# Kernel tuning notes

Measured on AMD Instinct MI355X. Metric: run time of the kernel, lower is better.

Reference implementation:

```python
import jax, jax.numpy as jnp
import numpy as np

B = 32768
STATE_DIM = 5
MEAS_DIM = 4
CTRL_DIM = 2
HIDDEN = 128
NOISE_HIDDEN = 64
DT = 0.01
Q_ENTR_LB = 7.1
N_SIG = 2 * STATE_DIM + 1
LAM = 3.0 - STATE_DIM          # merwe kappa = 3 - n, alpha = 1, beta = 0
C = STATE_DIM + LAM            # = 3.0


def _ukf_weights():
    wm = jnp.full((N_SIG,), 1.0 / (2.0 * C), dtype=jnp.float32)
    return wm.at[0].set(LAM / C)


def _sigma_points(x, P):
    # x: [B,n], P: [B,n,n] -> [B, 2n+1, n]
    L = jnp.linalg.cholesky(C * P)
    cols = jnp.swapaxes(L, -1, -2)  # row i is the i-th column of L
    return jnp.concatenate([x[:, None, :], x[:, None, :] + cols, x[:, None, :] - cols], axis=1)


def _dyn(xu, W1, b1, W2, b2):
    # ODE right-hand side on the augmented state xu: [B, S, state+ctrl]
    return jnp.tanh(xu @ W1 + b1) @ W2 + b2


def _rk4(xu, W1, b1, W2, b2):
    # single RK4 step over dt (odeint(model, xu, dt)[-1])
    f = lambda z: _dyn(z, W1, b1, W2, b2)
    k1 = f(xu)
    k2 = f(xu + 0.5 * DT * k1)
    k3 = f(xu + 0.5 * DT * k2)
    k4 = f(xu + DT * k3)
    return xu + (DT / 6.0) * (k1 + 2.0 * k2 + 2.0 * k3 + k4)


def _entropy(M):
    D = M.shape[-1]
    return 0.5 * D * (1.0 + jnp.log(2.0 * jnp.pi)) + 0.5 * jnp.linalg.slogdet(M)[1]


def setup_inputs() -> dict:
    key = jax.random.key(0)
    ks = jax.random.split(key, 12)
    d_in = STATE_DIM + CTRL_DIM
    X_hat = jax.random.normal(ks[0], (B, STATE_DIM), dtype=jnp.float32)
    A = 0.1 * jax.random.normal(ks[1], (B, STATE_DIM, STATE_DIM), dtype=jnp.float32)
    P = A @ jnp.swapaxes(A, -1, -2) + 0.1 * jnp.eye(STATE_DIM, dtype=jnp.float32)  # SPD
    u = jax.random.normal(ks[2], (B, CTRL_DIM), dtype=jnp.float32)
    y = jax.random.normal(ks[3], (B, MEAS_DIM), dtype=jnp.float32)
    W1 = 0.05 * jax.random.normal(ks[4], (d_in, HIDDEN), dtype=jnp.float32)
    b1 = jnp.zeros((HIDDEN,), dtype=jnp.float32)
    W2 = 0.05 * jax.random.normal(ks[5], (HIDDEN, d_in), dtype=jnp.float32)
    b2 = jnp.zeros((d_in,), dtype=jnp.float32)
    Wn1 = 0.05 * jax.random.normal(ks[6], (STATE_DIM, NOISE_HIDDEN), dtype=jnp.float32)
    bn1 = jnp.zeros((NOISE_HIDDEN,), dtype=jnp.float32)
    Wq = 0.05 * jax.random.normal(ks[7], (NOISE_HIDDEN, STATE_DIM), dtype=jnp.float32)
    bq = jnp.zeros((STATE_DIM,), dtype=jnp.float32)
    Wr = 0.05 * jax.random.normal(ks[8], (NOISE_HIDDEN, MEAS_DIM), dtype=jnp.float32)
    br = jnp.zeros((MEAS_DIM,), dtype=jnp.float32)
    Hobs = 0.3 * jax.random.normal(ks[9], (d_in, MEAS_DIM), dtype=jnp.float32)
    return {"X_hat": X_hat, "P": P, "u": u, "y": y,
            "W1": W1, "b1": b1, "W2": W2, "b2": b2,
            "Wn1": Wn1, "bn1": bn1, "Wq": Wq, "bq": bq, "Wr": Wr, "br": br,
            "Hobs": Hobs}


def reference(X_hat, P, u, y, W1, b1, W2, b2, Wn1, bn1, Wq, bq, Wr, br, Hobs):
    wm = _ukf_weights()
    wc = wm  # alpha=1, beta=0 -> Wc0 == Wm0
    # --- noise model: per-sample diagonal Q, R from a small MLP ---
    h = jnp.tanh(X_hat @ Wn1 + bn1)
    Q = jnp.eye(STATE_DIM, dtype=X_hat.dtype) * jnp.exp(h @ Wq + bq)[:, :, None]
    R = jnp.eye(MEAS_DIM, dtype=X_hat.dtype) * jnp.exp(h @ Wr + br)[:, :, None]
    # --- entropy projection on Q (boolean mask -> where) ---
    ent_q = _entropy(Q)
    scale = jnp.where(ent_q < Q_ENTR_LB, jnp.exp((Q_ENTR_LB - ent_q) / STATE_DIM), 1.0)
    Q = scale[:, None, None] * Q
    ur = jnp.broadcast_to(u[:, None, :], (u.shape[0], N_SIG, CTRL_DIM))
    # --- UKF predict ---
    pts = _sigma_points(X_hat, P)                       # [B,11,5]
    xu = jnp.concatenate([pts, ur], axis=-1)            # [B,11,7]
    pts_n = _rk4(xu, W1, b1, W2, b2)[..., :STATE_DIM]   # integrate, keep state dims
    x_pred = jnp.einsum('s,bsn->bn', wm, pts_n)
    d = pts_n - x_pred[:, None, :]
    P_pred = jnp.einsum('s,bsi,bsj->bij', wc, d, d) + Q
    # --- UKF update ---
    pts2 = _sigma_points(x_pred, P_pred)
    Y = jnp.concatenate([pts2, ur], axis=-1) @ Hobs     # [B,11,4]
    y_hat = jnp.einsum('s,bsm->bm', wm, Y)
    dy = Y - y_hat[:, None, :]
    S = jnp.einsum('s,bsi,bsj->bij', wc, dy, dy) + R
    dx = pts2 - x_pred[:, None, :]
    Pxy = jnp.einsum('s,bsi,bsj->bij', wc, dx, dy)
    # K = Pxy @ S^{-1}, via solve (S symmetric)
    K = jnp.swapaxes(jnp.linalg.solve(S, jnp.swapaxes(Pxy, -1, -2)), -1, -2)
    X_new = x_pred + jnp.einsum('bij,bj->bi', K, y - y_hat)
    P_new = P_pred - K @ S @ jnp.swapaxes(K, -1, -2)
    return (X_new, P_new, _entropy(Q), _entropy(R))
```

## Files before the change

kernel.cpp:

```cpp
#include <hip/hip_runtime.h>
#include <math.h>

#define B_N   32768
#define SD    5
#define MD    4
#define HID   128
#define NH    64
#define DT    0.01f

#define IDX(i, j) ((i) * ((i) + 1) / 2 + (j))

typedef _Float16 h2v  __attribute__((ext_vector_type(2)));
typedef float    f32x4 __attribute__((ext_vector_type(4)));

#define CONST_AS __attribute__((address_space(4)))

__device__ __forceinline__ f32x4 ldc4(const float* p) {
    return *(const CONST_AS f32x4*)(uintptr_t)p;
}

__device__ __forceinline__ float fexp2(float x) {
#if __has_builtin(__builtin_amdgcn_exp2f)
    return __builtin_amdgcn_exp2f(x);
#else
    return exp2f(x);
#endif
}

__device__ __forceinline__ float fexp(float x) {
    return fexp2(x * 1.4426950408889634f);
}

__device__ __forceinline__ float packh2(float a, float b) {
    union { h2v h; float f; } u;
    u.h.x = (_Float16)a; u.h.y = (_Float16)b;
    return u.f;
}
__device__ __forceinline__ float unpk_lo(float f) {
    union { float f; h2v h; } u; u.f = f; return (float)u.h.x;
}
__device__ __forceinline__ float unpk_hi(float f) {
    union { float f; h2v h; } u; u.f = f; return (float)u.h.y;
}
__device__ __forceinline__ float pk_neg(float f) {
    union { float f; unsigned u; } x; x.f = f; x.u ^= 0x80008000u; return x.f;
}

__device__ __forceinline__ float pk_fma_vs(float a, float b_s, float c) {
    float d;
    asm("v_pk_fma_f16 %0, %1, %2, %3" : "=v"(d) : "v"(a), "s"(b_s), "v"(c));
    return d;
}
__device__ __forceinline__ float pk_fma_vv(float a, float b, float c) {
    float d;
    asm("v_pk_fma_f16 %0, %1, %2, %3" : "=v"(d) : "v"(a), "v"(b), "v"(c));
    return d;
}
__device__ __forceinline__ float pk_mul(float a, float b) {
    float d;
    asm("v_pk_mul_f16 %0, %1, %2" : "=v"(d) : "v"(a), "v"(b));
    return d;
}
__device__ __forceinline__ float pk_mul_vs(float a, float b_s) {
    float d;
    asm("v_pk_mul_f16 %0, %1, %2" : "=v"(d) : "v"(a), "s"(b_s));
    return d;
}
__device__ __forceinline__ float pk_add(float a, float b) {
    float d;
    asm("v_pk_add_f16 %0, %1, %2" : "=v"(d) : "v"(a), "v"(b));
    return d;
}
__device__ __forceinline__ float pk_max(float a, float b) {
    float d;
    asm("v_pk_max_f16 %0, %1, %2" : "=v"(d) : "v"(a), "v"(b));
    return d;
}
__device__ __forceinline__ float pk_min(float a, float b) {
    float d;
    asm("v_pk_min_f16 %0, %1, %2" : "=v"(d) : "v"(a), "v"(b));
    return d;
}

__device__ __forceinline__ float pk_tanh(float pre) {
    const float PHIc = packh2(3.0f, 3.0f);
    const float PLOc = packh2(-3.0f, -3.0f);
    const float C4c  = packh2(0.000412619f, 0.000412619f);
    const float C3c  = packh2(-0.00901606f, -0.00901606f);
    const float C2c  = packh2(0.07293188f, 0.07293188f);
    const float C1c  = packh2(-0.30093534f, -0.30093534f);
    const float C0c  = packh2(0.9982018f, 0.9982018f);
    float pc = pk_min(pk_max(pre, PLOc), PHIc);
    float u = pk_mul(pc, pc);
    float h = pk_fma_vv(u, C4c, C3c);
    h = pk_fma_vv(u, h, C2c);
    h = pk_fma_vv(u, h, C1c);
    h = pk_fma_vv(u, h, C0c);
    return pk_mul(pc, h);
}

__global__ void ukf_prep(const float* __restrict__ W1, const float* __restrict__ b1,
                         const float* __restrict__ W2,
                         const float* __restrict__ Wn1, const float* __restrict__ bn1,
                         const float* __restrict__ Wq, const float* __restrict__ Wr,
                         float* __restrict__ wpk, float* __restrict__ wnk) {
    const int p = threadIdx.x;
    if (p < 64) {
        const int k0 = 2 * p, k1 = 2 * p + 1;
        float* o = wpk + p * 16;
#pragma unroll
        for (int i = 0; i < 7; ++i) o[i] = packh2(W1[i * HID + k0], W1[i * HID + k1]);
        o[7] = packh2(b1[k0], b1[k1]);
#pragma unroll
        for (int j = 0; j < 7; ++j) o[8 + j] = packh2(W2[k0 * 7 + j], W2[k1 * 7 + j]);
        o[15] = 0.0f;
    } else if (p < 96) {
        const int q = p - 64;
        const int k0 = 2 * q, k1 = 2 * q + 1;
        float* o = wnk + q * 16;
#pragma unroll
        for (int i = 0; i < 5; ++i) o[i] = packh2(Wn1[i * NH + k0], Wn1[i * NH + k1]);
        o[5] = packh2(bn1[k0], bn1[k1]);
#pragma unroll
        for (int j = 0; j < 5; ++j) o[6 + j] = packh2(Wq[k0 * 5 + j], Wq[k1 * 5 + j]);
#pragma unroll
        for (int j = 0; j < 4; ++j) o[11 + j] = packh2(Wr[k0 * 4 + j], Wr[k1 * 4 + j]);
        o[15] = 0.0f;
    }
}

#define PSTR 259
__global__ __launch_bounds__(640) void ukf_main(
    const float* __restrict__ Xh, const float* __restrict__ Pin,
    const float* __restrict__ Uin, const float* __restrict__ Yin,
    const float* __restrict__ b2g, const float* __restrict__ bqg,
    const float* __restrict__ brg, const float* __restrict__ Hg,
    const float* __restrict__ wpk, const float* __restrict__ wnk,
    float* __restrict__ out) {
    __shared__ float part[64 * PSTR];

    const int tid = threadIdx.x;
    const int role = tid >> 6;
    const int e = tid & 63;
    const int bb = blockIdx.x * 64 + e;

    float x[SD];
#pragma unroll
    for (int i = 0; i < SD; ++i) x[i] = Xh[bb * SD + i];

    if (role < 8) {
        const float u0 = Uin[bb * 2 + 0];
        const float u1 = Uin[bb * 2 + 1];
        float zb[7];
#pragma unroll
        for (int i = 0; i < SD; ++i) zb[i] = packh2(x[i], x[i]);
        zb[5] = packh2(u0, u0);
        zb[6] = packh2(u1, u1);
        const float ONE2 = packh2(1.0f, 1.0f);

        float fb[5];
        float J2[25];
#pragma unroll
        for (int i = 0; i < 5; ++i) fb[i] = 0.0f;
#pragma unroll
        for (int t = 0; t < 25; ++t) J2[t] = 0.0f;

        const int pbeg = role << 2;
#pragma unroll
        for (int pp = 0; pp < 4; ++pp) {
            const float* row = wpk + ((pbeg + pp) << 4);
            f32x4 wa = ldc4(row);
            f32x4 wb = ldc4(row + 4);
            f32x4 wc = ldc4(row + 8);
            f32x4 wd = ldc4(row + 12);
            float pre = pk_fma_vs(zb[0], wa.x, pk_mul_vs(ONE2, wb.w));
            pre = pk_fma_vs(zb[1], wa.y, pre);
            pre = pk_fma_vs(zb[2], wa.z, pre);
            pre = pk_fma_vs(zb[3], wa.w, pre);
            pre = pk_fma_vs(zb[4], wb.x, pre);
            pre = pk_fma_vs(zb[5], wb.y, pre);
            pre = pk_fma_vs(zb[6], wb.z, pre);
            float tt = pk_tanh(pre);
            fb[0] = pk_fma_vs(tt, wc.x, fb[0]);
            fb[1] = pk_fma_vs(tt, wc.y, fb[1]);
            fb[2] = pk_fma_vs(tt, wc.z, fb[2]);
            fb[3] = pk_fma_vs(tt, wc.w, fb[3]);
            fb[4] = pk_fma_vs(tt, wd.x, fb[4]);
            float t2 = pk_mul(tt, tt);
            float g2 = pk_add(ONE2, pk_neg(t2));
            float s0 = pk_mul_vs(g2, wa.x);
            float s1 = pk_mul_vs(g2, wa.y);
            float s2 = pk_mul_vs(g2, wa.z);
            float s3 = pk_mul_vs(g2, wa.w);
            float s4 = pk_mul_vs(g2, wb.x);
            float w2i[5] = { wc.x, wc.y, wc.z, wc.w, wd.x };
#pragma unroll
            for (int i = 0; i < 5; ++i) {
                J2[i * 5 + 0] = pk_fma_vs(s0, w2i[i], J2[i * 5 + 0]);
                J2[i * 5 + 1] = pk_fma_vs(s1, w2i[i], J2[i * 5 + 1]);
                J2[i * 5 + 2] = pk_fma_vs(s2, w2i[i], J2[i * 5 + 2]);
                J2[i * 5 + 3] = pk_fma_vs(s3, w2i[i], J2[i * 5 + 3]);
                J2[i * 5 + 4] = pk_fma_vs(s4, w2i[i], J2[i * 5 + 4]);
            }
        }
        float* o = part + e * PSTR + role * 30;
#pragma unroll
        for (int i = 0; i < 5; ++i) o[i] = fb[i];
#pragma unroll
        for (int t = 0; t < 25; ++t) o[5 + t] = J2[t];
    } else {
        const int w = role - 8;
        float xb[5];
#pragma unroll
        for (int i = 0; i < SD; ++i) xb[i] = packh2(x[i], x[i]);
        const float ONE2 = packh2(1.0f, 1.0f);
        float gq2[5] = {0.f, 0.f, 0.f, 0.f, 0.f};
        float gr2[4] = {0.f, 0.f, 0.f, 0.f};
        const int pbeg = w << 4;
#pragma unroll 4
        for (int pp = 0; pp < 16; ++pp) {
            const float* row = wnk + ((pbeg + pp) << 4);
            f32x4 wa = ldc4(row);
            f32x4 wb = ldc4(row + 4);
            f32x4 wc = ldc4(row + 8);
            f32x4 wd = ldc4(row + 12);
            float pre = pk_fma_vs(xb[0], wa.x, pk_mul_vs(ONE2, wb.y));
            pre = pk_fma_vs(xb[1], wa.y, pre);
            pre = pk_fma_vs(xb[2], wa.z, pre);
            pre = pk_fma_vs(xb[3], wa.w, pre);
            pre = pk_fma_vs(xb[4], wb.x, pre);
            float tt = pk_tanh(pre);
            gq2[0] = pk_fma_vs(tt, wb.z, gq2[0]);
            gq2[1] = pk_fma_vs(tt, wb.w, gq2[1]);
            gq2[2] = pk_fma_vs(tt, wc.x, gq2[2]);
            gq2[3] = pk_fma_vs(tt, wc.y, gq2[3]);
            gq2[4] = pk_fma_vs(tt, wc.z, gq2[4]);
            gr2[0] = pk_fma_vs(tt, wc.w, gr2[0]);
            gr2[1] = pk_fma_vs(tt, wd.x, gr2[1]);
            gr2[2] = pk_fma_vs(tt, wd.y, gr2[2]);
            gr2[3] = pk_fma_vs(tt, wd.z, gr2[3]);
        }
        float* o = part + e * PSTR + 240 + w * 9;
#pragma unroll
        for (int r = 0; r < 5; ++r) o[r] = gq2[r];
#pragma unroll
        for (int r = 0; r < 4; ++r) o[5 + r] = gr2[r];
    }

    __syncthreads();

    if (tid < 64) {
        const float* pe = part + tid * PSTR;

        float fb2[5], J2[25];
#pragma unroll
        for (int i = 0; i < 5; ++i) fb2[i] = pe[i];
#pragma unroll
        for (int t = 0; t < 25; ++t) J2[t] = pe[5 + t];
#pragma unroll
        for (int r = 1; r < 8; ++r) {
            const float* pr = pe + r * 30;
#pragma unroll
            for (int i = 0; i < 5; ++i) fb2[i] = pk_add(fb2[i], pr[i]);
#pragma unroll
            for (int t = 0; t < 25; ++t) J2[t] = pk_add(J2[t], pr[5 + t]);
        }

        float xp[SD];
#pragma unroll
        for (int i = 0; i < SD; ++i)
            xp[i] = x[i] + DT * (b2g[i] + unpk_lo(fb2[i]) + unpk_hi(fb2[i]));

        float A[5][5];
#pragma unroll
        for (int i = 0; i < 5; ++i)
#pragma unroll
            for (int j = 0; j < 5; ++j)
                A[i][j] = ((i == j) ? 1.0f : 0.0f)
                        + DT * (unpk_lo(J2[i * 5 + j]) + unpk_hi(J2[i * 5 + j]));

        float Pf[5][5];
#pragma unroll
        for (int i = 0; i < 5; ++i)
#pragma unroll
            for (int j = 0; j < 5; ++j) Pf[i][j] = Pin[bb * 25 + i * 5 + j];
        float T[5][5];
#pragma unroll
        for (int i = 0; i < 5; ++i)
#pragma unroll
            for (int l = 0; l < 5; ++l) {
                float v = 0.0f;
#pragma unroll
                for (int j = 0; j < 5; ++j) v = fmaf(A[i][j], Pf[j][l], v);
                T[i][l] = v;
            }
        float Pp[15];
#pragma unroll
        for (int i = 0; i < 5; ++i)
#pragma unroll
            for (int j = 0; j <= i; ++j) {
                float v = 0.0f;
#pragma unroll
                for (int l = 0; l < 5; ++l) v = fmaf(T[i][l], A[j][l], v);
                Pp[IDX(i, j)] = v;
            }

        float gq[5], gr[4];
#pragma unroll
        for (int r = 0; r < 5; ++r) {
            float s = pk_add(pe[240 + r], pe[240 + 9 + r]);
            gq[r] = bqg[r] + unpk_lo(s) + unpk_hi(s);
        }
#pragma unroll
        for (int r = 0; r < 4; ++r) {
            float s = pk_add(pe[240 + 5 + r], pe[240 + 14 + r]);
            gr[r] = brg[r] + unpk_lo(s) + unpk_hi(s);
        }

        const float ent0 = 7.0946927f + 0.5f * (gq[0] + gq[1] + gq[2] + gq[3] + gq[4]);
        const float logscale = fmaxf(7.1f - ent0, 0.0f) * 0.2f;
        const float entQ = fmaf(2.5f, logscale, ent0);
        const float entR = 5.6757541f + 0.5f * (gr[0] + gr[1] + gr[2] + gr[3]);
        float qd[5], rd[4];
#pragma unroll
        for (int j = 0; j < 5; ++j) qd[j] = fexp(gq[j] + logscale);
#pragma unroll
        for (int j = 0; j < 4; ++j) rd[j] = fexp(gr[j]);

#pragma unroll
        for (int j = 0; j < SD; ++j) Pp[IDX(j, j)] += qd[j];

        float Hh[7][4];
#pragma unroll
        for (int i = 0; i < 7; ++i)
#pragma unroll
            for (int m = 0; m < 4; ++m) Hh[i][m] = Hg[i * 4 + m];

        const float uu0 = Uin[bb * 2 + 0];
        const float uu1 = Uin[bb * 2 + 1];
        float yv[4];
#pragma unroll
        for (int m = 0; m < 4; ++m) yv[m] = Yin[bb * 4 + m];

        float yh[4];
#pragma unroll
        for (int m = 0; m < 4; ++m) {
            float v = fmaf(uu0, Hh[5][m], uu1 * Hh[6][m]);
#pragma unroll
            for (int i = 0; i < SD; ++i) v = fmaf(xp[i], Hh[i][m], v);
            yh[m] = v;
        }

        float Pxy[5][4];
#pragma unroll
        for (int i = 0; i < SD; ++i)
#pragma unroll
            for (int m = 0; m < 4; ++m) {
                float v = 0.0f;
#pragma unroll
                for (int j = 0; j < SD; ++j) {
                    float pij = (i >= j) ? Pp[IDX(i, j)] : Pp[IDX(j, i)];
                    v = fmaf(pij, Hh[j][m], v);
                }
                Pxy[i][m] = v;
            }

        float Sm[10];
#pragma unroll
        for (int m = 0; m < 4; ++m)
#pragma unroll
            for (int n = 0; n <= m; ++n) {
                float v = 0.0f;
#pragma unroll
                for (int i = 0; i < SD; ++i) v = fmaf(Hh[i][m], Pxy[i][n], v);
                Sm[IDX(m, n)] = v;
            }
#pragma unroll
        for (int m = 0; m < 4; ++m) Sm[IDX(m, m)] += rd[m];

        float Ls[10], di[4];
#pragma unroll
        for (int m = 0; m < 4; ++m) {
            float d = Sm[IDX(m, m)];
#pragma unroll
            for (int k = 0; k < m; ++k) { float l = Ls[IDX(m, k)]; d = fmaf(-l, l, d); }
            d = sqrtf(d);
            Ls[IDX(m, m)] = d;
            di[m] = 1.0f / d;
#pragma unroll
            for (int n = m + 1; n < 4; ++n) {
                float v = Sm[IDX(n, m)];
#pragma unroll
                for (int k = 0; k < m; ++k) v = fmaf(-Ls[IDX(n, k)], Ls[IDX(m, k)], v);
                Ls[IDX(n, m)] = v * di[m];
            }
        }

        float K[5][4];
#pragma unroll
        for (int i = 0; i < SD; ++i) {
            float w[4];
#pragma unroll
            for (int m = 0; m < 4; ++m) {
                float v = Pxy[i][m];
#pragma unroll
                for (int k = 0; k < m; ++k) v = fmaf(-Ls[IDX(m, k)], w[k], v);
                w[m] = v * di[m];
            }
#pragma unroll
            for (int m = 3; m >= 0; --m) {
                float v = w[m];
#pragma unroll
                for (int k = m + 1; k < 4; ++k) v = fmaf(-Ls[IDX(k, m)], K[i][k], v);
                K[i][m] = v * di[m];
            }
        }

        float inn[4];
#pragma unroll
        for (int m = 0; m < 4; ++m) inn[m] = yv[m] - yh[m];

        float Xn[5];
#pragma unroll
        for (int i = 0; i < SD; ++i) {
            float v = xp[i];
#pragma unroll
            for (int m = 0; m < 4; ++m) v = fmaf(K[i][m], inn[m], v);
            Xn[i] = v;
        }

        float KS[5][4];
#pragma unroll
        for (int i = 0; i < SD; ++i)
#pragma unroll
            for (int m = 0; m < 4; ++m) {
                float v = 0.0f;
#pragma unroll
                for (int n = 0; n < 4; ++n) {
                    float snm = (n >= m) ? Sm[IDX(n, m)] : Sm[IDX(m, n)];
                    v = fmaf(K[i][n], snm, v);
                }
                KS[i][m] = v;
            }
        float Pn[15];
#pragma unroll
        for (int i = 0; i < SD; ++i)
#pragma unroll
            for (int j = 0; j <= i; ++j) {
                float v = Pp[IDX(i, j)];
#pragma unroll
                for (int m = 0; m < 4; ++m) v = fmaf(-KS[i][m], K[j][m], v);
                Pn[IDX(i, j)] = v;
            }

#pragma unroll
        for (int i = 0; i < SD; ++i) out[bb * SD + i] = Xn[i];
        float* Po = out + B_N * SD + bb * 25;
#pragma unroll
        for (int i = 0; i < SD; ++i)
#pragma unroll
            for (int j = 0; j < SD; ++j)
                Po[i * 5 + j] = (i >= j) ? Pn[IDX(i, j)] : Pn[IDX(j, i)];
        out[B_N * 30 + bb] = entQ;
        out[B_N * 31 + bb] = entR;
    }
}

extern "C" void kernel_launch(void* const* d_in, const int* in_sizes, int n_in,
                              void* d_out, int out_size, void* d_ws, size_t ws_size,
                              hipStream_t stream) {
    const float* Xh  = (const float*)d_in[0];
    const float* P   = (const float*)d_in[1];
    const float* u   = (const float*)d_in[2];
    const float* y   = (const float*)d_in[3];
    const float* W1  = (const float*)d_in[4];
    const float* b1  = (const float*)d_in[5];
    const float* W2  = (const float*)d_in[6];
    const float* b2  = (const float*)d_in[7];
    const float* Wn1 = (const float*)d_in[8];
    const float* bn1 = (const float*)d_in[9];
    const float* Wq  = (const float*)d_in[10];
    const float* bq  = (const float*)d_in[11];
    const float* Wr  = (const float*)d_in[12];
    const float* br  = (const float*)d_in[13];
    const float* Hob = (const float*)d_in[14];

    float* wpk = (float*)d_ws;
    float* wnk = wpk + 64 * 16;

    ukf_prep<<<1, 128, 0, stream>>>(W1, b1, W2, Wn1, bn1, Wq, Wr, wpk, wnk);
    ukf_main<<<B_N / 64, 640, 0, stream>>>(Xh, P, u, y, b2, bq, br, Hob,
                                           wpk, wnk, (float*)d_out);
}
```

Measured before the change: 99.01 us.

## Fuse weight packing into main kernel and read packed weights from LDS

Removes the separate prep kernel launch and instead has each block pack the fp16 weight pairs into shared memory, then synchronize before the MLP phase. Weight reads switch from scalar constant loads (SGPR operands) to LDS vector loads feeding VGPR operands. This saves a launch and the global workspace round-trip, but every block now redoes the packing from global memory, adds a barrier, uses more LDS, and replaces the scalar-broadcast weights with LDS reads and extra VGPR pressure.

New measurement: 95.82 us. 1.03x faster.

```diff
diff --git a/kernel.cpp b/kernel.cpp
--- a/kernel.cpp
+++ b/kernel.cpp
@@ -13,12 +13,6 @@
 typedef _Float16 h2v  __attribute__((ext_vector_type(2)));
 typedef float    f32x4 __attribute__((ext_vector_type(4)));
 
-#define CONST_AS __attribute__((address_space(4)))
-
-__device__ __forceinline__ f32x4 ldc4(const float* p) {
-    return *(const CONST_AS f32x4*)(uintptr_t)p;
-}
-
 __device__ __forceinline__ float fexp2(float x) {
 #if __has_builtin(__builtin_amdgcn_exp2f)
     return __builtin_amdgcn_exp2f(x);
@@ -46,11 +40,6 @@
     union { float f; unsigned u; } x; x.f = f; x.u ^= 0x80008000u; return x.f;
 }
 
-__device__ __forceinline__ float pk_fma_vs(float a, float b_s, float c) {
-    float d;
-    asm("v_pk_fma_f16 %0, %1, %2, %3" : "=v"(d) : "v"(a), "s"(b_s), "v"(c));
-    return d;
-}
 __device__ __forceinline__ float pk_fma_vv(float a, float b, float c) {
     float d;
     asm("v_pk_fma_f16 %0, %1, %2, %3" : "=v"(d) : "v"(a), "v"(b), "v"(c));
@@ -59,11 +48,6 @@
 __device__ __forceinline__ float pk_mul(float a, float b) {
     float d;
     asm("v_pk_mul_f16 %0, %1, %2" : "=v"(d) : "v"(a), "v"(b));
-    return d;
-}
-__device__ __forceinline__ float pk_mul_vs(float a, float b_s) {
-    float d;
-    asm("v_pk_mul_f16 %0, %1, %2" : "=v"(d) : "v"(a), "s"(b_s));
     return d;
 }
 __device__ __forceinline__ float pk_add(float a, float b) {
@@ -99,44 +83,19 @@
     return pk_mul(pc, h);
 }
 
-__global__ void ukf_prep(const float* __restrict__ W1, const float* __restrict__ b1,
-                         const float* __restrict__ W2,
-                         const float* __restrict__ Wn1, const float* __restrict__ bn1,
-                         const float* __restrict__ Wq, const float* __restrict__ Wr,
-                         float* __restrict__ wpk, float* __restrict__ wnk) {
-    const int p = threadIdx.x;
-    if (p < 64) {
-        const int k0 = 2 * p, k1 = 2 * p + 1;
-        float* o = wpk + p * 16;
-#pragma unroll
-        for (int i = 0; i < 7; ++i) o[i] = packh2(W1[i * HID + k0], W1[i * HID + k1]);
-        o[7] = packh2(b1[k0], b1[k1]);
-#pragma unroll
-        for (int j = 0; j < 7; ++j) o[8 + j] = packh2(W2[k0 * 7 + j], W2[k1 * 7 + j]);
-        o[15] = 0.0f;
-    } else if (p < 96) {
-        const int q = p - 64;
-        const int k0 = 2 * q, k1 = 2 * q + 1;
-        float* o = wnk + q * 16;
-#pragma unroll
-        for (int i = 0; i < 5; ++i) o[i] = packh2(Wn1[i * NH + k0], Wn1[i * NH + k1]);
-        o[5] = packh2(bn1[k0], bn1[k1]);
-#pragma unroll
-        for (int j = 0; j < 5; ++j) o[6 + j] = packh2(Wq[k0 * 5 + j], Wq[k1 * 5 + j]);
-#pragma unroll
-        for (int j = 0; j < 4; ++j) o[11 + j] = packh2(Wr[k0 * 4 + j], Wr[k1 * 4 + j]);
-        o[15] = 0.0f;
-    }
-}
-
 #define PSTR 259
 __global__ __launch_bounds__(640) void ukf_main(
     const float* __restrict__ Xh, const float* __restrict__ Pin,
     const float* __restrict__ Uin, const float* __restrict__ Yin,
-    const float* __restrict__ b2g, const float* __restrict__ bqg,
-    const float* __restrict__ brg, const float* __restrict__ Hg,
-    const float* __restrict__ wpk, const float* __restrict__ wnk,
+    const float* __restrict__ W1, const float* __restrict__ b1,
+    const float* __restrict__ W2, const float* __restrict__ b2g,
+    const float* __restrict__ Wn1, const float* __restrict__ bn1,
+    const float* __restrict__ Wq, const float* __restrict__ bqg,
+    const float* __restrict__ Wr, const float* __restrict__ brg,
+    const float* __restrict__ Hg,
     float* __restrict__ out) {
+    __shared__ __align__(16) float swp[64 * 16];
+    __shared__ __align__(16) float swn[32 * 16];
     __shared__ float part[64 * PSTR];
 
     const int tid = threadIdx.x;
@@ -144,9 +103,34 @@
     const int e = tid & 63;
     const int bb = blockIdx.x * 64 + e;
 
+    if (tid < 64) {
+        const int k0 = 2 * tid, k1 = 2 * tid + 1;
+        float* o = swp + tid * 16;
+#pragma unroll
+        for (int i = 0; i < 7; ++i) o[i] = packh2(W1[i * HID + k0], W1[i * HID + k1]);
+        o[7] = packh2(b1[k0], b1[k1]);
+#pragma unroll
+        for (int j = 0; j < 7; ++j) o[8 + j] = packh2(W2[k0 * 7 + j], W2[k1 * 7 + j]);
+        o[15] = 0.0f;
+    } else if (tid < 96) {
+        const int q = tid - 64;
+        const int k0 = 2 * q, k1 = 2 * q + 1;
+        float* o = swn + q * 16;
+#pragma unroll
+        for (int i = 0; i < 5; ++i) o[i] = packh2(Wn1[i * NH + k0], Wn1[i * NH + k1]);
+        o[5] = packh2(bn1[k0], bn1[k1]);
+#pragma unroll
+        for (int j = 0; j < 5; ++j) o[6 + j] = packh2(Wq[k0 * 5 + j], Wq[k1 * 5 + j]);
+#pragma unroll
+        for (int j = 0; j < 4; ++j) o[11 + j] = packh2(Wr[k0 * 4 + j], Wr[k1 * 4 + j]);
+        o[15] = 0.0f;
+    }
+
     float x[SD];
 #pragma unroll
     for (int i = 0; i < SD; ++i) x[i] = Xh[bb * SD + i];
+
+    __syncthreads();
 
     if (role < 8) {
         const float u0 = Uin[bb * 2 + 0];
@@ -168,39 +152,39 @@
         const int pbeg = role << 2;
 #pragma unroll
         for (int pp = 0; pp < 4; ++pp) {
-            const float* row = wpk + ((pbeg + pp) << 4);
-            f32x4 wa = ldc4(row);
-            f32x4 wb = ldc4(row + 4);
-            f32x4 wc = ldc4(row + 8);
-            f32x4 wd = ldc4(row + 12);
-            float pre = pk_fma_vs(zb[0], wa.x, pk_mul_vs(ONE2, wb.w));
-            pre = pk_fma_vs(zb[1], wa.y, pre);
-            pre = pk_fma_vs(zb[2], wa.z, pre);
-            pre = pk_fma_vs(zb[3], wa.w, pre);
-            pre = pk_fma_vs(zb[4], wb.x, pre);
-            pre = pk_fma_vs(zb[5], wb.y, pre);
-            pre = pk_fma_vs(zb[6], wb.z, pre);
+            const float* row = swp + ((pbeg + pp) << 4);
+            f32x4 wa = *(const f32x4*)(row);
+            f32x4 wb = *(const f32x4*)(row + 4);
+            f32x4 wc = *(const f32x4*)(row + 8);
+            f32x4 wd = *(const f32x4*)(row + 12);
+            float pre = pk_fma_vv(zb[0], wa.x, wb.w);
+            pre = pk_fma_vv(zb[1], wa.y, pre);
+            pre = pk_fma_vv(zb[2], wa.z, pre);
+            pre = pk_fma_vv(zb[3], wa.w, pre);
+            pre = pk_fma_vv(zb[4], wb.x, pre);
+            pre = pk_fma_vv(zb[5], wb.y, pre);
+            pre = pk_fma_vv(zb[6], wb.z, pre);
             float tt = pk_tanh(pre);
-            fb[0] = pk_fma_vs(tt, wc.x, fb[0]);
-            fb[1] = pk_fma_vs(tt, wc.y, fb[1]);
-            fb[2] = pk_fma_vs(tt, wc.z, fb[2]);
-            fb[3] = pk_fma_vs(tt, wc.w, fb[3]);
-            fb[4] = pk_fma_vs(tt, wd.x, fb[4]);
+            fb[0] = pk_fma_vv(tt, wc.x, fb[0]);
+            fb[1] = pk_fma_vv(tt, wc.y, fb[1]);
+            fb[2] = pk_fma_vv(tt, wc.z, fb[2]);
+            fb[3] = pk_fma_vv(tt, wc.w, fb[3]);
+            fb[4] = pk_fma_vv(tt, wd.x, fb[4]);
             float t2 = pk_mul(tt, tt);
             float g2 = pk_add(ONE2, pk_neg(t2));
-            float s0 = pk_mul_vs(g2, wa.x);
-            float s1 = pk_mul_vs(g2, wa.y);
-            float s2 = pk_mul_vs(g2, wa.z);
-            float s3 = pk_mul_vs(g2, wa.w);
-            float s4 = pk_mul_vs(g2, wb.x);
+            float s0 = pk_mul(g2, wa.x);
+            float s1 = pk_mul(g2, wa.y);
+            float s2 = pk_mul(g2, wa.z);
+            float s3 = pk_mul(g2, wa.w);
+            float s4 = pk_mul(g2, wb.x);
             float w2i[5] = { wc.x, wc.y, wc.z, wc.w, wd.x };
 #pragma unroll
             for (int i = 0; i < 5; ++i) {
-                J2[i * 5 + 0] = pk_fma_vs(s0, w2i[i], J2[i * 5 + 0]);
-                J2[i * 5 + 1] = pk_fma_vs(s1, w2i[i], J2[i * 5 + 1]);
-                J2[i * 5 + 2] = pk_fma_vs(s2, w2i[i], J2[i * 5 + 2]);
-                J2[i * 5 + 3] = pk_fma_vs(s3, w2i[i], J2[i * 5 + 3]);
-                J2[i * 5 + 4] = pk_fma_vs(s4, w2i[i], J2[i * 5 + 4]);
+                J2[i * 5 + 0] = pk_fma_vv(s0, w2i[i], J2[i * 5 + 0]);
+                J2[i * 5 + 1] = pk_fma_vv(s1, w2i[i], J2[i * 5 + 1]);
+                J2[i * 5 + 2] = pk_fma_vv(s2, w2i[i], J2[i * 5 + 2]);
+                J2[i * 5 + 3] = pk_fma_vv(s3, w2i[i], J2[i * 5 + 3]);
+                J2[i * 5 + 4] = pk_fma_vv(s4, w2i[i], J2[i * 5 + 4]);
             }
         }
         float* o = part + e * PSTR + role * 30;
@@ -213,32 +197,31 @@
         float xb[5];
 #pragma unroll
         for (int i = 0; i < SD; ++i) xb[i] = packh2(x[i], x[i]);
-        const float ONE2 = packh2(1.0f, 1.0f);
         float gq2[5] = {0.f, 0.f, 0.f, 0.f, 0.f};
         float gr2[4] = {0.f, 0.f, 0.f, 0.f};
         const int pbeg = w << 4;
 #pragma unroll 4
         for (int pp = 0; pp < 16; ++pp) {
-            const float* row = wnk + ((pbeg + pp) << 4);
-            f32x4 wa = ldc4(row);
-            f32x4 wb = ldc4(row + 4);
-            f32x4 wc = ldc4(row + 8);
-            f32x4 wd = ldc4(row + 12);
-            float pre = pk_fma_vs(xb[0], wa.x, pk_mul_vs(ONE2, wb.y));
-            pre = pk_fma_vs(xb[1], wa.y, pre);
-            pre = pk_fma_vs(xb[2], wa.z, pre);
-            pre = pk_fma_vs(xb[3], wa.w, pre);
-            pre = pk_fma_vs(xb[4], wb.x, pre);
+            const float* row = swn + ((pbeg + pp) << 4);
+            f32x4 wa = *(const f32x4*)(row);
+            f32x4 wb = *(const f32x4*)(row + 4);
+            f32x4 wc = *(const f32x4*)(row + 8);
+            f32x4 wd = *(const f32x4*)(row + 12);
+            float pre = pk_fma_vv(xb[0], wa.x, wb.y);
+            pre = pk_fma_vv(xb[1], wa.y, pre);
+            pre = pk_fma_vv(xb[2], wa.z, pre);
+            pre = pk_fma_vv(xb[3], wa.w, pre);
+            pre = pk_fma_vv(xb[4], wb.x, pre);
             float tt = pk_tanh(pre);
-            gq2[0] = pk_fma_vs(tt, wb.z, gq2[0]);
-            gq2[1] = pk_fma_vs(tt, wb.w, gq2[1]);
-            gq2[2] = pk_fma_vs(tt, wc.x, gq2[2]);
-            gq2[3] = pk_fma_vs(tt, wc.y, gq2[3]);
-            gq2[4] = pk_fma_vs(tt, wc.z, gq2[4]);
-            gr2[0] = pk_fma_vs(tt, wc.w, gr2[0]);
-            gr2[1] = pk_fma_vs(tt, wd.x, gr2[1]);
-            gr2[2] = pk_fma_vs(tt, wd.y, gr2[2]);
-            gr2[3] = pk_fma_vs(tt, wd.z, gr2[3]);
+            gq2[0] = pk_fma_vv(tt, wb.z, gq2[0]);
+            gq2[1] = pk_fma_vv(tt, wb.w, gq2[1]);
+            gq2[2] = pk_fma_vv(tt, wc.x, gq2[2]);
+            gq2[3] = pk_fma_vv(tt, wc.y, gq2[3]);
+            gq2[4] = pk_fma_vv(tt, wc.z, gq2[4]);
+            gr2[0] = pk_fma_vv(tt, wc.w, gr2[0]);
+            gr2[1] = pk_fma_vv(tt, wd.x, gr2[1]);
+            gr2[2] = pk_fma_vv(tt, wd.y, gr2[2]);
+            gr2[3] = pk_fma_vv(tt, wd.z, gr2[3]);
         }
         float* o = part + e * PSTR + 240 + w * 9;
 #pragma unroll
@@ -485,10 +468,8 @@
     const float* br  = (const float*)d_in[13];
     const float* Hob = (const float*)d_in[14];
 
-    float* wpk = (float*)d_ws;
-    float* wnk = wpk + 64 * 16;
-
-    ukf_prep<<<1, 128, 0, stream>>>(W1, b1, W2, Wn1, bn1, Wq, Wr, wpk, wnk);
-    ukf_main<<<B_N / 64, 640, 0, stream>>>(Xh, P, u, y, b2, bq, br, Hob,
-                                           wpk, wnk, (float*)d_out);
-}
+    ukf_main<<<B_N / 64, 640, 0, stream>>>(Xh, P, u, y,
+                                           W1, b1, W2, b2,
+                                           Wn1, bn1, Wq, bq, Wr, br,
+                                           Hob, (float*)d_out);
+}
```
